# Kernel tuning notes

Hardware: AMD Instinct MI355X
Metric: run time of the kernel (lower is better)

The kernel has to match this reference:

```python
import jax, jax.numpy as jnp
from jax import lax
import numpy as np

B, H, W = 8, 352, 1216
CLIPVARIANCE = 5.0   # init kwarg
MAXRANGE = 32        # init kwarg

# 1-pixel shifts with zero padding. out[...,m,n] = x at the shifted location.
def s_pos_w(x):  # out[..., n] = x[..., n-1]
    return jnp.pad(x[..., :, :-1], ((0, 0), (0, 0), (0, 0), (1, 0)))

def s_neg_w(x):  # out[..., n] = x[..., n+1]
    return jnp.pad(x[..., :, 1:], ((0, 0), (0, 0), (0, 0), (0, 1)))

def s_pos_h(x):  # out[..., m, :] = x[..., m-1, :]
    return jnp.pad(x[..., :-1, :], ((0, 0), (0, 0), (1, 0), (0, 0)))

def s_neg_h(x):  # out[..., m, :] = x[..., m+1, :]
    return jnp.pad(x[..., 1:, :], ((0, 0), (0, 0), (0, 1), (0, 0)))


def _dir_accumulate(shift, logstep, depthin, maskf, var_d):
    """Scan outward up to MAXRANGE steps in one direction, accumulating
    confidence weights exp(-min(var, clip)) and variance-weighted depth
    hypotheses depth[src] * exp(integrated log-gradient along the path).
    Paths break at the first unmasked pixel (valid is a running product)."""
    z = jnp.zeros_like(depthin)

    def body(carry, _):
        valid, c, dsh, vsh, aw, awd = carry
        valid = shift(valid * maskf)          # path contiguity
        c = logstep(c)                         # integrated log-depth ratio
        dsh = shift(dsh)                       # source-pixel depth
        vsh = shift(vsh)                       # source-pixel variance
        w = jnp.exp(-jnp.minimum(vsh, CLIPVARIANCE)) * valid
        aw = aw + w
        awd = awd + w * jnp.exp(c) * dsh
        return (valid, c, dsh, vsh, aw, awd), None

    init = (jnp.ones_like(depthin), z, depthin, var_d, z, z)
    (_, _, _, _, aw, awd), _ = lax.scan(body, init, None, length=MAXRANGE)
    return aw, awd


def crf_lateralre(pred_log, mask, variance, depthin):
    """One 4-direction variance-weighted CRF integration pass."""
    maskf = mask.astype(depthin.dtype)
    plog_h = pred_log[:, 0:1]  # log d[m,n+1] - log d[m,n]
    plog_v = pred_log[:, 1:2]  # log d[m+1,n] - log d[m,n]

    dirs = [
        (s_pos_w, lambda c: s_pos_w(c + plog_h), variance[:, 0:1]),  # from left
        (s_neg_w, lambda c: s_neg_w(c) - plog_h, variance[:, 1:2]),  # from right
        (s_pos_h, lambda c: s_pos_h(c + plog_v), variance[:, 2:3]),  # from above
        (s_neg_h, lambda c: s_neg_h(c) - plog_v, variance[:, 3:4]),  # from below
    ]

    tot_w = jnp.zeros_like(depthin)
    tot_wd = jnp.zeros_like(depthin)
    for shift, logstep, var_d in dirs:
        aw, awd = _dir_accumulate(shift, logstep, depthin, maskf, var_d)
        tot_w = tot_w + aw
        tot_wd = tot_wd + awd

    lateralre = jnp.where(tot_w > 0, tot_wd / jnp.maximum(tot_w, 1e-12), 0.0)
    return lateralre * maskf


def setup_inputs() -> dict:
    key = jax.random.key(0)
    k1, k2, k3, k4 = jax.random.split(key, 4)
    pred_log = jax.random.normal(k1, (B, 2, H, W), jnp.float32) * 0.05
    mask = (jax.random.uniform(k2, (B, 1, H, W)) < 0.9).astype(jnp.int32)
    variance = jax.random.uniform(k3, (B, 4, H, W), jnp.float32) * 8.0
    depthin = jax.random.uniform(k4, (B, 1, H, W), jnp.float32) * 10.0 + 1.0
    lam = jnp.array([0.2], jnp.float32)
    return {"pred_log": pred_log, "mask": mask, "variance": variance,
            "depthin": depthin, "lam": lam, "times": 1}


def reference(pred_log, mask, variance, depthin, lam, times):
    depthout = depthin
    for _ in range(times):
        lateralre = crf_lateralre(pred_log, mask, variance, depthout)
        sel = (lateralre > 0).astype(depthin.dtype)
        depthout = (1 - sel) * depthin + sel * (depthin * (1 - lam) + lateralre * lam)
    return depthout
```

## Files before the change

### kernel.cpp

```cpp
#include <hip/hip_runtime.h>
#include <stdint.h>

#define HH 352
#define WW 1216
#define HW (HH*WW)
#define BB 8
#define CLIPV 5.0f
#define MAXR 32

#define VR 22
#define NBAND (HH/VR)
#define PFD 8
#define TOT (VR + MAXR)

template<int DIR>
__device__ __forceinline__ void vert_scan(
    const int* __restrict__ m, const float* __restrict__ plog_v,
    const float* __restrict__ vp, const float* __restrict__ d,
    const int w, const int h0, const int lane,
    float2 (&obuf0)[VR][64], float (&obw)[VR], float (&obq)[VR])
{
    const int hs   = DIR ? (h0 + VR - 1 + MAXR) : (h0 - MAXR);
    const int step = DIR ? -1 : 1;

    float rq_q[VR], rq_w[VR];
    int   r_mi[PFD];
    float r_pl[PFD], r_vv[PFD], r_dd[PFD];

    #pragma unroll
    for (int p = 0; p < PFD; ++p) {
        int hp = hs + p * step;
        int hc = min(max(hp, 0), HH-1);
        int idx = hc * WW + w;
        r_mi[p] = m[idx];
        r_pl[p] = plog_v[idx];
        r_vv[p] = vp[idx];
        r_dd[p] = d[idx];
    }

    float Q = 0.f, W = 0.f, EG = 1.f;
    int last_inv = hs - step;

    #pragma unroll
    for (int it = 0; it < TOT; ++it) {
        const int h  = hs + it * step;
        const int sl = it % PFD;

        int   mi  = ((unsigned)h < (unsigned)HH) ? r_mi[sl] : 0;
        float pl  = r_pl[sl];
        float vvx = r_vv[sl];
        float dd  = r_dd[sl];

        if (it + PFD < TOT) {
            int hp = h + PFD * step;
            int hc = min(max(hp, 0), HH-1);
            int idx = hc * WW + w;
            r_mi[sl] = m[idx];
            r_pl[sl] = plog_v[idx];
            r_vv[sl] = vp[idx];
            r_dd[sl] = d[idx];
        }

        bool  res = (mi == 0);
        float g   = __expf(pl);
        float wt  = __expf(-fminf(vvx, CLIPV));
        float q, outw, outq;
        if constexpr (DIR == 0) {
            outw = W; outq = EG * Q;
            q = wt * dd * __builtin_amdgcn_rcpf(EG);
            Q  = res ? 0.f : (Q + q);
            W  = res ? 0.f : (W + wt);
            EG = res ? 1.f : (EG * g);
        } else {
            float EDh = EG * g;
            outw = W; outq = Q * __builtin_amdgcn_rcpf(EDh);
            q = wt * dd * EDh;
            Q  = res ? 0.f : (Q + q);
            W  = res ? 0.f : (W + wt);
            EG = res ? 1.f : EDh;
        }
        last_inv = res ? h : last_inv;

        if (it >= MAXR) {
            if constexpr (DIR == 0) obuf0[it - MAXR][lane] = make_float2(outw, outq);
            else { obw[VR - 1 - (it - MAXR)] = outw; obq[VR - 1 - (it - MAXR)] = outq; }
        }
        if (it < VR) { rq_q[it] = q; rq_w[it] = wt; }
        if (it >= MAXR) {
            int s_out = h - MAXR * step;
            bool alive = DIR ? (s_out < last_inv) : (s_out > last_inv);
            Q -= alive ? rq_q[it - MAXR] : 0.f;
            W -= alive ? rq_w[it - MAXR] : 0.f;
        }
    }
}

__global__ __launch_bounds__(128) void crf_vert(
    const float* __restrict__ pred_log, const int* __restrict__ mask,
    const float* __restrict__ variance, const float* __restrict__ depth,
    float2* __restrict__ vq)
{
    __shared__ float2 obuf0[VR][64];

    const int lane = threadIdx.x & 63;
    const int dir  = threadIdx.x >> 6;
    const int id   = blockIdx.x;
    const int xcd  = id & 7;
    const int seq  = id >> 3;
    const int wc   = seq % 19;
    const int t2   = seq / 19;
    const int band = xcd * 2 + (t2 & 1);
    const int b    = t2 >> 1;
    const int w    = wc * 64 + lane;

    const float* plog_v = pred_log + ((size_t)b*2 + 1) * HW;
    const int*   m  = mask     + (size_t)b*HW;
    const float* vp = variance + ((size_t)b*4 + (dir ? 3 : 2)) * HW;
    const float* d  = depth    + (size_t)b*HW;

    const int h0 = band * VR;

    float obw[VR], obq[VR];

    if (dir == 0) {
        vert_scan<0>(m, plog_v, vp, d, w, h0, lane, obuf0, obw, obq);
    } else {
        vert_scan<1>(m, plog_v, vp, d, w, h0, lane, obuf0, obw, obq);
    }

    __syncthreads();
    if (dir == 1) {
        float2* pvq = vq + (size_t)b*HW;
        const int w0 = wc * 64;
        #pragma unroll
        for (int r = 0; r < VR; ++r) {
            float2 a = obuf0[r][lane];
            pvq[(h0 + r) * WW + w0 + lane] = make_float2(a.x + obw[r], a.y + obq[r]);
        }
    }
}

__global__ __launch_bounds__(256) void crf_horiz(
    const float* __restrict__ pred_log, const int* __restrict__ mask,
    const float* __restrict__ variance, const float* __restrict__ depth,
    const float* __restrict__ lam_p,
    const float2* __restrict__ vq,
    float* __restrict__ out)
{
    __shared__ float sG[WW];
    __shared__ float sH[WW];
    __shared__ float sI[WW];
    __shared__ float sJ[WW];
    __shared__ float sEt[19], sEti[19], sTw0[19], sTq0[19];
    __shared__ unsigned long long sBal[19];

    const int tid  = threadIdx.x;
    const int lane = tid & 63;
    const int wv   = tid >> 6;
    const int i    = blockIdx.x;
    const int h    = (i & 7) * 44 + (i >> 3);
    const int b    = blockIdx.y;

    const float* plrow = pred_log + (size_t)b*2*HW + h*WW;
    const int*   mrow  = mask     + (size_t)b*HW   + h*WW;
    const float* v0row = variance + (size_t)b*4*HW + h*WW;
    const float* v1row = v0row + HW;
    const float* drow  = depth    + (size_t)b*HW   + h*WW;
    const float2* vqrow= vq  + (size_t)b*HW + h*WW;
    float*       orow  = out + (size_t)b*HW + h*WW;

    float l_pAx[5], l_xw0[5], l_xq0[5], l_iw1[5], l_iq1[5], l_m[5], l_d[5];

    #pragma unroll
    for (int r = 0; r < 5; ++r) {
        int c = r*4 + wv;
        if (c < 19) {
            int j = c*64 + lane;
            float pl  = plrow[j];
            int   mi  = mrow[j];
            float dj  = drow[j];
            float wt0 = __expf(-fminf(v0row[j], CLIPV));
            float wt1 = __expf(-fminf(v1row[j], CLIPV));
            float ipA = pl;
            #pragma unroll
            for (int dlt = 1; dlt < 64; dlt <<= 1) {
                float u = __shfl_up(ipA, dlt, 64);
                if (lane >= dlt) ipA += u;
            }
            float pAx = ipA - pl;
            float S   = __shfl(ipA, 63, 64);
            float Einv = __expf(-pAx);
            float q0 = wt0 * dj * Einv;
            float q1 = wt1 * dj * Einv;
            float iw0 = wt0, iq0 = q0, iw1 = wt1, iq1 = q1;
            #pragma unroll
            for (int dlt = 1; dlt < 64; dlt <<= 1) {
                float a = __shfl_up(iw0, dlt, 64);
                float e = __shfl_up(iq0, dlt, 64);
                float f = __shfl_up(iw1, dlt, 64);
                float g = __shfl_up(iq1, dlt, 64);
                if (lane >= dlt) { iw0 += a; iq0 += e; iw1 += f; iq1 += g; }
            }
            sG[j] = iw0 - wt0;
            sH[j] = iq0 - q0;
            sI[j] = iw1;
            sJ[j] = iq1;
            unsigned long long bal = __ballot(mi == 0);
            if (lane == 63) {
                sEt[c]  = __expf(S);
                sEti[c] = __expf(-S);
                sTw0[c] = iw0;
                sTq0[c] = iq0;
            }
            if (lane == 0) sBal[c] = bal;
            l_pAx[r] = pAx; l_xw0[r] = iw0 - wt0; l_xq0[r] = iq0 - q0;
            l_iw1[r] = iw1; l_iq1[r] = iq1;
            l_m[r] = (float)mi; l_d[r] = dj;
        }
    }
    __syncthreads();

    const float lam = lam_p[0];

    #pragma unroll
    for (int r = 0; r < 5; ++r) {
        int c = r*4 + wv;
        if (c < 19) {
            const int c0 = c*64;
            const int j  = c0 + lane;
            float E = __expf(l_pAx[r]);
            unsigned long long balOwn = sBal[c];
            unsigned long long mb = balOwn & ((1ull << lane) - 1ull);
            int lm = mb ? (c0 + 63 - __builtin_clzll(mb)) : -1;
            if (c > 0 && lane < 32) {
                unsigned long long mp = sBal[c-1] & ~((1ull << (lane + 32)) - 1ull);
                if (mp) { int lm2 = c0 - 64 + 63 - __builtin_clzll(mp); lm = max(lm, lm2); }
            }
            int a0 = max(j - MAXR, lm + 1);
            float W0, Q0;
            if (a0 >= c0) {
                W0 = l_xw0[r] - sG[a0];
                Q0 = E * (l_xq0[r] - sH[a0]);
            } else {
                W0 = l_xw0[r] + (sTw0[c-1] - sG[a0]);
                Q0 = E * l_xq0[r] + E * sEt[c-1] * (sTq0[c-1] - sH[a0]);
            }
            int nm = 1 << 30;
            if (lane < 63) {
                unsigned long long nb = balOwn >> (lane + 1);
                if (nb) nm = j + 1 + __builtin_ctzll(nb);
            }
            if (c < 18 && lane >= 32) {
                unsigned long long nn = sBal[c+1] & ((1ull << (lane - 31)) - 1ull);
                if (nn) nm = min(nm, c0 + 64 + (int)__builtin_ctzll(nn));
            }
            int b1 = min(j + MAXR, nm - 1);
            b1 = min(b1, WW - 1);
            int endin = min(b1, c0 + 63);
            float W1 = 0.f, Q1 = 0.f;
            if (endin > j) {
                W1 = sI[endin] - l_iw1[r];
                Q1 = E * (sJ[endin] - l_iq1[r]);
            }
            if (b1 > c0 + 63) {
                W1 += sI[b1];
                Q1 += E * sEti[c] * sJ[b1];
            }
            float2 vt = vqrow[j];
            float totw  = W0 + W1 + vt.x;
            float totwd = Q0 + Q1 + vt.y;
            float lat = (totw > 0.f) ? (totwd / fmaxf(totw, 1e-12f)) : 0.f;
            lat *= l_m[r];
            float dj = l_d[r];
            orow[j] = (lat > 0.f) ? (dj * (1.f - lam) + lat * lam) : dj;
        }
    }
}

#define BWF 256
#define PADF 32
#define LWF (BWF + 2*PADF)

__global__ __launch_bounds__(256) void crf_fallback(
    const float* __restrict__ pred_log, const int* __restrict__ mask,
    const float* __restrict__ variance, const float* __restrict__ depth,
    const float* __restrict__ lam_p, float* __restrict__ out)
{
    __shared__ float s_m[LWF], s_wt0[LWF], s_wt1[LWF], s_gh[LWF], s_ghi[LWF], s_d[LWF];
    const int t  = threadIdx.x;
    const int i  = blockIdx.x;
    const int h  = (i & 7) * 44 + (i >> 3);
    const int w0 = blockIdx.y * BWF;
    const int b  = blockIdx.z;
    const float* plog_h = pred_log + (size_t)b * 2 * HW;
    const float* plog_v = plog_h + HW;
    const int*   m      = mask   + (size_t)b * HW;
    const float* v0     = variance + (size_t)b * 4 * HW;
    const float* v1     = v0 + HW;
    const float* v2     = v0 + 2 * HW;
    const float* v3     = v0 + 3 * HW;
    const float* d      = depth + (size_t)b * HW;
    for (int j = t; j < LWF; j += BWF) {
        int gw = w0 - PADF + j;
        float mf=0.f, wt0=0.f, wt1=0.f, gh=1.f, ghi=1.f, dd=0.f;
        if (gw >= 0 && gw < WW) {
            int idx = h * WW + gw;
            mf = (float)m[idx];
            float pl = plog_h[idx];
            gh = __expf(pl); ghi = __expf(-pl);
            wt0 = __expf(-fminf(v0[idx], CLIPV));
            wt1 = __expf(-fminf(v1[idx], CLIPV));
            dd = d[idx];
        }
        s_m[j]=mf; s_wt0[j]=wt0; s_wt1[j]=wt1; s_gh[j]=gh; s_ghi[j]=ghi; s_d[j]=dd;
    }
    __syncthreads();
    const int w = w0 + t;
    if (w >= WW) return;
    const int c = t + PADF;
    float totw = 0.f, totwd = 0.f;
    { float e=1.f, valid=1.f;
      #pragma unroll 8
      for (int k=1;k<=MAXR;++k){int s=c-k; valid*=s_m[s]; e*=s_gh[s];
        float wgt=s_wt0[s]*valid; totw+=wgt; totwd+=wgt*e*s_d[s];} }
    { float e=1.f, valid=1.f;
      #pragma unroll 8
      for (int k=1;k<=MAXR;++k){int s=c+k; e*=s_ghi[s-1]; valid*=s_m[s];
        float wgt=s_wt1[s]*valid; totw+=wgt; totwd+=wgt*e*s_d[s];} }
    { const int kup=min(MAXR,h); float e=1.f, valid=1.f;
      #pragma unroll 4
      for (int k=1;k<=kup;++k){int idx=(h-k)*WW+w; valid*=(float)m[idx];
        e*=__expf(plog_v[idx]); float wgt=__expf(-fminf(v2[idx],CLIPV))*valid;
        totw+=wgt; totwd+=wgt*e*d[idx];} }
    { const int kdn=min(MAXR,HH-1-h); float e=1.f, valid=1.f;
      #pragma unroll 4
      for (int k=1;k<=kdn;++k){int idx=(h+k)*WW+w; e*=__expf(-plog_v[idx-WW]);
        valid*=(float)m[idx]; float wgt=__expf(-fminf(v3[idx],CLIPV))*valid;
        totw+=wgt; totwd+=wgt*e*d[idx];} }
    const int base = h * WW + w;
    float lat = (totw > 0.f) ? (totwd / fmaxf(totw, 1e-12f)) : 0.f;
    lat *= s_m[c];
    float lam = lam_p[0];
    float di  = s_d[c];
    out[(size_t)b * HW + base] = (lat > 0.f) ? (di * (1.f - lam) + lat * lam) : di;
}

extern "C" void kernel_launch(void* const* d_in, const int* in_sizes, int n_in,
                              void* d_out, int out_size, void* d_ws, size_t ws_size,
                              hipStream_t stream) {
    const float* pred_log = (const float*)d_in[0];
    const int*   mask     = (const int*)  d_in[1];
    const float* variance = (const float*)d_in[2];
    const float* depthin  = (const float*)d_in[3];
    const float* lam      = (const float*)d_in[4];
    float* out = (float*)d_out;

    const size_t need = (size_t)BB * HW * sizeof(float2);
    if (ws_size >= need) {
        float2* vq = (float2*)d_ws;
        dim3 vgrid(19 * NBAND * BB, 1, 1);
        hipLaunchKernelGGL(crf_vert, vgrid, dim3(128), 0, stream,
                           pred_log, mask, variance, depthin, vq);
        dim3 hgrid(HH, BB);
        hipLaunchKernelGGL(crf_horiz, hgrid, dim3(256), 0, stream,
                           pred_log, mask, variance, depthin, lam, vq, out);
    } else {
        dim3 fgrid(HH, (WW + BWF - 1) / BWF, BB);
        hipLaunchKernelGGL(crf_fallback, fgrid, dim3(BWF), 0, stream,
                           pred_log, mask, variance, depthin, lam, out);
    }
}
```

Measured before the change: 182.3 us.

## Double vertical band height and merge directions via LDS atomic adds

Vertical band size goes from 22 to 44 rows. The ratio of the 32-row warm-up halo to useful rows drops, so fewer redundant reloads and scan steps are spent per output row. The sliding-window history becomes a 32-entry ring buffer. Both direction wavefronts now add their outputs into a zeroed shared buffer with workgroup-scope atomics instead of holding per-thread register arrays, and both wavefronts split the final store. This halves the grid (8 bands per batch) and adds LDS atomic traffic in exchange.

```diff
diff --git a/kernel.cpp b/kernel.cpp
--- a/kernel.cpp
+++ b/kernel.cpp
@@ -8,22 +8,26 @@
 #define CLIPV 5.0f
 #define MAXR 32
 
-#define VR 22
+#define VR 44
 #define NBAND (HH/VR)
 #define PFD 8
 #define TOT (VR + MAXR)
+
+__device__ __forceinline__ void lds_fadd(float* p, float v) {
+    __hip_atomic_fetch_add(p, v, __ATOMIC_RELAXED, __HIP_MEMORY_SCOPE_WORKGROUP);
+}
 
 template<int DIR>
 __device__ __forceinline__ void vert_scan(
     const int* __restrict__ m, const float* __restrict__ plog_v,
     const float* __restrict__ vp, const float* __restrict__ d,
     const int w, const int h0, const int lane,
-    float2 (&obuf0)[VR][64], float (&obw)[VR], float (&obq)[VR])
+    float2 (&obuf0)[VR][64])
 {
     const int hs   = DIR ? (h0 + VR - 1 + MAXR) : (h0 - MAXR);
     const int step = DIR ? -1 : 1;
 
-    float rq_q[VR], rq_w[VR];
+    float rq_q[MAXR], rq_w[MAXR];
     int   r_mi[PFD];
     float r_pl[PFD], r_vv[PFD], r_dd[PFD];
 
@@ -82,16 +86,17 @@
         last_inv = res ? h : last_inv;
 
         if (it >= MAXR) {
-            if constexpr (DIR == 0) obuf0[it - MAXR][lane] = make_float2(outw, outq);
-            else { obw[VR - 1 - (it - MAXR)] = outw; obq[VR - 1 - (it - MAXR)] = outq; }
-        }
-        if (it < VR) { rq_q[it] = q; rq_w[it] = wt; }
+            const int r = DIR ? (VR - 1 - (it - MAXR)) : (it - MAXR);
+            lds_fadd(&obuf0[r][lane].x, outw);
+            lds_fadd(&obuf0[r][lane].y, outq);
+        }
         if (it >= MAXR) {
             int s_out = h - MAXR * step;
             bool alive = DIR ? (s_out < last_inv) : (s_out > last_inv);
-            Q -= alive ? rq_q[it - MAXR] : 0.f;
-            W -= alive ? rq_w[it - MAXR] : 0.f;
-        }
+            Q -= alive ? rq_q[it & (MAXR-1)] : 0.f;
+            W -= alive ? rq_w[it & (MAXR-1)] : 0.f;
+        }
+        if (it < VR) { rq_q[it & (MAXR-1)] = q; rq_w[it & (MAXR-1)] = wt; }
     }
 }
 
@@ -105,12 +110,10 @@
     const int lane = threadIdx.x & 63;
     const int dir  = threadIdx.x >> 6;
     const int id   = blockIdx.x;
-    const int xcd  = id & 7;
+    const int band = id & 7;
     const int seq  = id >> 3;
     const int wc   = seq % 19;
-    const int t2   = seq / 19;
-    const int band = xcd * 2 + (t2 & 1);
-    const int b    = t2 >> 1;
+    const int b    = seq / 19;
     const int w    = wc * 64 + lane;
 
     const float* plog_v = pred_log + ((size_t)b*2 + 1) * HW;
@@ -120,22 +123,25 @@
 
     const int h0 = band * VR;
 
-    float obw[VR], obq[VR];
+    #pragma unroll
+    for (int r2 = 0; r2 < VR/2; ++r2)
+        obuf0[dir*(VR/2) + r2][lane] = make_float2(0.f, 0.f);
+    __syncthreads();
 
     if (dir == 0) {
-        vert_scan<0>(m, plog_v, vp, d, w, h0, lane, obuf0, obw, obq);
+        vert_scan<0>(m, plog_v, vp, d, w, h0, lane, obuf0);
     } else {
-        vert_scan<1>(m, plog_v, vp, d, w, h0, lane, obuf0, obw, obq);
+        vert_scan<1>(m, plog_v, vp, d, w, h0, lane, obuf0);
     }
 
     __syncthreads();
-    if (dir == 1) {
+    {
         float2* pvq = vq + (size_t)b*HW;
-        const int w0 = wc * 64;
+        const int w0c = wc * 64;
         #pragma unroll
-        for (int r = 0; r < VR; ++r) {
-            float2 a = obuf0[r][lane];
-            pvq[(h0 + r) * WW + w0 + lane] = make_float2(a.x + obw[r], a.y + obq[r]);
+        for (int r2 = 0; r2 < VR/2; ++r2) {
+            int r = dir*(VR/2) + r2;
+            pvq[(h0 + r) * WW + w0c + lane] = obuf0[r][lane];
         }
     }
 }
```

New measurement: 230.1 us. 1.26x slower.
